# Optimization experiments

Measured on AMD Instinct MI355X. Metric: run time of the kernel, lower is better.

The kernel has to match this reference:

```python
import jax, jax.numpy as jnp
import numpy as np

B, C, T, V, P = 32, 64, 512, 54, 4
EPS = 1e-5


def setup_inputs() -> dict:
    key = jax.random.key(0)
    ks = jax.random.split(key, 5)
    x = jax.random.normal(ks[0], (B, C, T, V), dtype=jnp.float32)
    A = jax.random.uniform(ks[1], (P, V, V), dtype=jnp.float32)
    gweights = jax.random.normal(ks[2], (P, V, V), dtype=jnp.float32)
    W = jax.random.normal(ks[3], (P, C, C), dtype=jnp.float32) * 0.05  # (P, C_out, C_in)
    b = jax.random.normal(ks[4], (P, C), dtype=jnp.float32) * 0.05
    gamma = jnp.ones((C,), dtype=jnp.float32)
    beta = jnp.zeros((C,), dtype=jnp.float32)
    return {"x": x, "A": A, "gweights": gweights, "W": W, "b": b,
            "gamma": gamma, "beta": beta}


def reference(x, A, gweights, W, b, gamma, beta):
    # x: (B, C_in, T, V)
    Aeff = A * gweights  # (P, V, V), learned-weighted adjacency
    # per-part graph aggregation (x @ A_p) followed by 1x1 conv, summed over parts
    # out[b,o,t,v] = sum_p sum_c sum_u x[b,c,t,u] * Aeff[p,u,v] * W[p,o,c] + sum_p b[p,o]
    y = jnp.einsum('bctu,puv,poc->botv', x, Aeff, W, optimize=True)
    y = y + jnp.sum(b, axis=0)[None, :, None, None]
    # BatchNorm2d in training mode: batch stats over (B, T, V) per channel
    mean = jnp.mean(y, axis=(0, 2, 3), keepdims=True)
    var = jnp.mean(jnp.square(y - mean), axis=(0, 2, 3), keepdims=True)
    y = (y - mean) * jax.lax.rsqrt(var + EPS)
    y = y * gamma[None, :, None, None] + beta[None, :, None, None]
    y = jax.nn.relu(y)
    # temporal_conv is Identity (kernel_size=None); residual shortcut is Identity (C_in==C_out)
    return y + x
```

## Files before the change

### kernel.cpp

```cpp
#include <hip/hip_runtime.h>
#include <hip/hip_bf16.h>


typedef __bf16 bf16_t;
typedef __bf16 bf16x8 __attribute__((ext_vector_type(8)));
typedef __bf16 bf16x4 __attribute__((ext_vector_type(4)));
typedef float  f32x4  __attribute__((ext_vector_type(4)));
typedef unsigned int uint32;

static __device__ __forceinline__ f32x4 mfma16(bf16x8 a, bf16x8 b, f32x4 c) {
  return __builtin_amdgcn_mfma_f32_16x16x32_bf16(a, b, c, 0, 0, 0);
}
static __device__ __forceinline__ uint32 pk2(float a, float b) {
  union { __bf16 h; unsigned short u; } ua, ub;
  ua.h = (__bf16)a; ub.h = (__bf16)b;
  return (uint32)ua.u | ((uint32)ub.u << 16);
}

#define XTOT 56623104ull

__global__ __launch_bounds__(256) void k_prep(
    const float* __restrict__ A, const float* __restrict__ g,
    const float* __restrict__ W, const float* __restrict__ bias,
    bf16_t* __restrict__ W2, bf16_t* __restrict__ Ae,
    float* __restrict__ bsum, float* __restrict__ stats) {
  int i = blockIdx.x * 256 + threadIdx.x;
  if (i < 16384) {
    int o = i >> 8, k = i & 255, p = k >> 6, c = k & 63;
    W2[i] = (bf16_t)W[p * 4096 + o * 64 + c];
  }
  if (i < 224 * 64) {
    int pv = i >> 6, u = i & 63;
    int p = pv / 56, v = pv - p * 56;
    float val = 0.f;
    if (v < 54 && u < 54) {
      int idx = (p * 54 + u) * 54 + v;
      val = A[idx] * g[idx];
    }
    Ae[i] = (bf16_t)val;
  }
  if (i < 64) {
    float s = 0.f;
    for (int p = 0; p < 4; ++p) s += bias[p * 64 + i];
    bsum[i] = s;
  }
  if (i < 8192) stats[i] = 0.f;
}

#define ZS  264
#define XSS 72

template<bool YBF16>
__global__ __launch_bounds__(256, 3) void k_pass1(
    const float* __restrict__ x, const bf16_t* __restrict__ W2,
    const bf16_t* __restrict__ Ae, const float* __restrict__ bsum,
    void* __restrict__ yprev, float* __restrict__ stats) {
  __shared__ bf16_t Zt[64 * ZS];
  __shared__ bf16_t Xs[64 * XSS];

  const int tid  = threadIdx.x;
  const int bid  = blockIdx.x;
  const int b    = bid >> 7;
  const int t0   = (bid & 127) << 2;
  const int w    = tid >> 6;
  const int L    = tid & 63;
  const int quad = L >> 4;
  const int l15  = L & 15;

  for (int i = tid; i < 8 * ZS / 2; i += 256)
    ((uint32*)(Zt + 56 * ZS))[i] = 0u;

  bf16x8 wf[8];
  #pragma unroll
  for (int kk = 0; kk < 8; ++kk)
    wf[kk] = *(const bf16x8*)(W2 + (((w << 4) + l15) << 8) + (kk << 5) + (quad << 3));

  int zoff[14];
  #pragma unroll
  for (int n = 0; n < 14; ++n) {
    int pv = (n << 4) + l15;
    int p = pv / 56;
    int v = pv - p * 56;
    zoff[n] = v * ZS + (p << 6) + (w << 4) + (quad << 2);
  }

  const int oc  = (w << 4) + l15;
  const float bsv = bsum[oc];
  float ssum = 0.f, ssq = 0.f;

  const size_t LIM   = XTOT - 2;
  const size_t gbase = ((size_t)(b << 6) + (tid >> 5)) * 27648 + ((size_t)(tid & 31) << 1);
  uint32* xsd = (uint32*)((char*)Xs + (tid >> 5) * (XSS * 2) + ((tid & 31) << 2));

  float2 pf[8];
  #pragma unroll
  for (int j = 0; j < 8; ++j) {
    size_t a = gbase + (size_t)j * 221184 + (size_t)t0 * 54;
    if (a > LIM) a = LIM;
    pf[j] = *(const float2*)(x + a);
  }

  for (int tt = 0; tt < 4; ++tt) {
    const int t = t0 + tt;

    #pragma unroll
    for (int j = 0; j < 8; ++j) xsd[j * 288] = pk2(pf[j].x, pf[j].y);

    if (tt < 3) {
      #pragma unroll
      for (int j = 0; j < 8; ++j) {
        size_t a = gbase + (size_t)j * 221184 + (size_t)(t + 1) * 54;
        if (a > LIM) a = LIM;
        pf[j] = *(const float2*)(x + a);
      }
    }

    __syncthreads();

    const bf16_t* xr = Xs + oc * XSS;
    bf16x8 xa0 = *(const bf16x8*)(xr + (quad << 3));
    bf16x8 xa1 = *(const bf16x8*)(xr + 32 + (quad << 3));
    #pragma unroll
    for (int n = 0; n < 14; ++n) {
      const bf16_t* ar = Ae + (((n << 4) + l15) << 6) + (quad << 3);
      f32x4 acc = {0.f, 0.f, 0.f, 0.f};
      acc = mfma16(xa0, *(const bf16x8*)(ar), acc);
      acc = mfma16(xa1, *(const bf16x8*)(ar + 32), acc);
      uint32* dst = (uint32*)(Zt + zoff[n]);
      dst[0] = pk2(acc[0], acc[1]);
      dst[1] = pk2(acc[2], acc[3]);
    }

    __syncthreads();

    const size_t obase = (((size_t)((b << 6) + oc) << 9) + (size_t)t) * 54;
    #pragma unroll
    for (int mi = 0; mi < 4; ++mi) {
      f32x4 acc = {0.f, 0.f, 0.f, 0.f};
      #pragma unroll
      for (int kk = 0; kk < 8; ++kk) {
        bf16x8 za = *(const bf16x8*)(Zt + ((mi << 4) + l15) * ZS
                                        + (kk << 5) + (quad << 3));
        acc = mfma16(za, wf[kk], acc);
      }
      const int v0 = (mi << 4) + (quad << 2);
      if (v0 + 3 < 54) {
        float y0 = acc[0] + bsv, y1 = acc[1] + bsv, y2 = acc[2] + bsv, y3 = acc[3] + bsv;
        if (YBF16) {
          uint32* d = (uint32*)((bf16_t*)yprev + obase + v0);
          d[0] = pk2(y0, y1); d[1] = pk2(y2, y3);
        } else {
          float2* d = (float2*)((float*)yprev + obase + v0);
          d[0] = make_float2(y0, y1); d[1] = make_float2(y2, y3);
        }
        ssum += y0 + y1 + y2 + y3;
        ssq  += y0 * y0 + y1 * y1 + y2 * y2 + y3 * y3;
      } else if (v0 == 52) {
        float y0 = acc[0] + bsv, y1 = acc[1] + bsv;
        if (YBF16) {
          *(uint32*)((bf16_t*)yprev + obase + v0) = pk2(y0, y1);
        } else {
          *(float2*)((float*)yprev + obase + v0) = make_float2(y0, y1);
        }
        ssum += y0 + y1;
        ssq  += y0 * y0 + y1 * y1;
      }
    }
  }

  ssum += __shfl_xor(ssum, 16); ssq += __shfl_xor(ssq, 16);
  ssum += __shfl_xor(ssum, 32); ssq += __shfl_xor(ssq, 32);
  if (L < 16) {
    float* sb = stats + (bid & 63) * 128;
    atomicAdd(&sb[oc], ssum);
    atomicAdd(&sb[64 + oc], ssq);
  }
}

__global__ void k_finalize(const float* __restrict__ gamma, const float* __restrict__ beta,
                           const float* __restrict__ stats, float* __restrict__ ac) {
  int o = threadIdx.x;
  if (o >= 64) return;
  float S = 0.f, Q = 0.f;
  for (int buf = 0; buf < 64; ++buf) {
    S += stats[buf * 128 + o];
    Q += stats[buf * 128 + 64 + o];
  }
  const float inv = 1.0f / 884736.0f;
  float mean = S * inv;
  float var  = Q * inv - mean * mean;
  float a = gamma[o] * rsqrtf(var + 1e-5f);
  ac[o] = a;
  ac[64 + o] = beta[o] - mean * a;
}

template<bool YBF16>
__global__ __launch_bounds__(256) void k_pass2(const float* __restrict__ x,
                                               const float* __restrict__ ac,
                                               const void* __restrict__ yprev,
                                               float* __restrict__ out) {
  const int slab = blockIdx.y;
  const int o = slab & 63;
  const size_t base = (size_t)slab * 27648 + (size_t)(((blockIdx.x << 8) + threadIdx.x) << 2);
  const float a = ac[o], c = ac[64 + o];
  float y0, y1, y2, y3;
  if (YBF16) {
    bf16x4 yp = *(const bf16x4*)((const bf16_t*)yprev + base);
    y0 = (float)yp[0]; y1 = (float)yp[1]; y2 = (float)yp[2]; y3 = (float)yp[3];
  } else {
    float4 yp = *(const float4*)((const float*)yprev + base);
    y0 = yp.x; y1 = yp.y; y2 = yp.z; y3 = yp.w;
  }
  float4 xv = *(const float4*)(x + base);
  float4 r;
  r.x = fmaxf(fmaf(a, y0, c), 0.f) + xv.x;
  r.y = fmaxf(fmaf(a, y1, c), 0.f) + xv.y;
  r.z = fmaxf(fmaf(a, y2, c), 0.f) + xv.z;
  r.w = fmaxf(fmaf(a, y3, c), 0.f) + xv.w;
  *(float4*)(out + base) = r;
}

extern "C" void kernel_launch(void* const* d_in, const int* in_sizes, int n_in,
                              void* d_out, int out_size, void* d_ws, size_t ws_size,
                              hipStream_t stream) {
  const float* x     = (const float*)d_in[0];
  const float* A     = (const float*)d_in[1];
  const float* g     = (const float*)d_in[2];
  const float* W     = (const float*)d_in[3];
  const float* bias  = (const float*)d_in[4];
  const float* gamma = (const float*)d_in[5];
  const float* beta  = (const float*)d_in[6];

  char* ws = (char*)d_ws;
  bf16_t* W2    = (bf16_t*)(ws + 0);
  bf16_t* Ae    = (bf16_t*)(ws + 32768);
  float*  bsum  = (float*)(ws + 61440);
  float*  stats = (float*)(ws + 61696);
  float*  ac    = (float*)(ws + 94464);
  const size_t YP_OFF   = 98304;
  const size_t YP_BYTES = (size_t)32 * 64 * 512 * 54 * 2;
  float* out = (float*)d_out;

  k_prep<<<64, 256, 0, stream>>>(A, g, W, bias, W2, Ae, bsum, stats);

  if (ws_size >= YP_OFF + YP_BYTES + 4096) {
    bf16_t* ypre = (bf16_t*)(ws + YP_OFF);
    k_pass1<true><<<4096, 256, 0, stream>>>(x, W2, Ae, bsum, ypre, stats);
    k_finalize<<<1, 64, 0, stream>>>(gamma, beta, stats, ac);
    k_pass2<true><<<dim3(27, 2048), 256, 0, stream>>>(x, ac, ypre, out);
  } else {
    k_pass1<false><<<4096, 256, 0, stream>>>(x, W2, Ae, bsum, out, stats);
    k_finalize<<<1, 64, 0, stream>>>(gamma, beta, stats, ac);
    k_pass2<false><<<dim3(27, 2048), 256, 0, stream>>>(x, ac, out, out);
  }
}
```

Measured before the change: 757.8 us.

## Stage bf16 pre-norm output in LDS and write it block-contiguous

Pass1 now collects each timestep's bf16 pre-BN output in a shared tile and writes it to the workspace as one contiguous block-ordered chunk with 16-byte stores, instead of scattered 8-byte stores across channel rows. Pass2 is rewritten to read that block-linear layout contiguously and to gather x and scatter out by index, with the BN coefficients cached in LDS. The x prefetch now masks out the idle lanes instead of clamping addresses, and it is issued after the second barrier rather than before the first. The aim is better coalescing of the intermediate traffic. The cost is an extra barrier per timestep, integer divides in pass2, and strided 8-byte accesses to x and out there.

```diff
diff --git a/kernel.cpp b/kernel.cpp
--- a/kernel.cpp
+++ b/kernel.cpp
@@ -16,8 +16,12 @@
   ua.h = (__bf16)a; ub.h = (__bf16)b;
   return (uint32)ua.u | ((uint32)ub.u << 16);
 }
-
-#define XTOT 56623104ull
+static __device__ __forceinline__ float bflo(uint32 u) {
+  union { uint32 u; float f; } r; r.u = u << 16; return r.f;
+}
+static __device__ __forceinline__ float bfhi(uint32 u) {
+  union { uint32 u; float f; } r; r.u = u & 0xffff0000u; return r.f;
+}
 
 __global__ __launch_bounds__(256) void k_prep(
     const float* __restrict__ A, const float* __restrict__ g,
@@ -57,6 +61,7 @@
     void* __restrict__ yprev, float* __restrict__ stats) {
   __shared__ bf16_t Zt[64 * ZS];
   __shared__ bf16_t Xs[64 * XSS];
+  __shared__ __align__(16) bf16_t Ys[64 * 54];
 
   const int tid  = threadIdx.x;
   const int bid  = blockIdx.x;
@@ -88,16 +93,18 @@
   const float bsv = bsum[oc];
   float ssum = 0.f, ssq = 0.f;
 
-  const size_t LIM   = XTOT - 2;
-  const size_t gbase = ((size_t)(b << 6) + (tid >> 5)) * 27648 + ((size_t)(tid & 31) << 1);
-  uint32* xsd = (uint32*)((char*)Xs + (tid >> 5) * (XSS * 2) + ((tid & 31) << 2));
+  const int  f2   = tid & 31;
+  const bool ldon = f2 < 27;
+  const size_t gbase = ((size_t)(b << 6) + (tid >> 5)) * 27648 + ((size_t)f2 << 1);
+  uint32* xsd = (uint32*)((char*)Xs + (tid >> 5) * (XSS * 2) + (f2 << 2));
 
   float2 pf[8];
   #pragma unroll
-  for (int j = 0; j < 8; ++j) {
-    size_t a = gbase + (size_t)j * 221184 + (size_t)t0 * 54;
-    if (a > LIM) a = LIM;
-    pf[j] = *(const float2*)(x + a);
+  for (int j = 0; j < 8; ++j) pf[j] = make_float2(0.f, 0.f);
+  if (ldon) {
+    #pragma unroll
+    for (int j = 0; j < 8; ++j)
+      pf[j] = *(const float2*)(x + gbase + (size_t)j * 221184 + (size_t)t0 * 54);
   }
 
   for (int tt = 0; tt < 4; ++tt) {
@@ -105,15 +112,6 @@
 
     #pragma unroll
     for (int j = 0; j < 8; ++j) xsd[j * 288] = pk2(pf[j].x, pf[j].y);
-
-    if (tt < 3) {
-      #pragma unroll
-      for (int j = 0; j < 8; ++j) {
-        size_t a = gbase + (size_t)j * 221184 + (size_t)(t + 1) * 54;
-        if (a > LIM) a = LIM;
-        pf[j] = *(const float2*)(x + a);
-      }
-    }
 
     __syncthreads();
 
@@ -132,6 +130,12 @@
     }
 
     __syncthreads();
+
+    if (ldon && tt < 3) {
+      #pragma unroll
+      for (int j = 0; j < 8; ++j)
+        pf[j] = *(const float2*)(x + gbase + (size_t)j * 221184 + (size_t)(t + 1) * 54);
+    }
 
     const size_t obase = (((size_t)((b << 6) + oc) << 9) + (size_t)t) * 54;
     #pragma unroll
@@ -147,7 +151,7 @@
       if (v0 + 3 < 54) {
         float y0 = acc[0] + bsv, y1 = acc[1] + bsv, y2 = acc[2] + bsv, y3 = acc[3] + bsv;
         if (YBF16) {
-          uint32* d = (uint32*)((bf16_t*)yprev + obase + v0);
+          uint32* d = (uint32*)(Ys + oc * 54 + v0);
           d[0] = pk2(y0, y1); d[1] = pk2(y2, y3);
         } else {
           float2* d = (float2*)((float*)yprev + obase + v0);
@@ -158,13 +162,23 @@
       } else if (v0 == 52) {
         float y0 = acc[0] + bsv, y1 = acc[1] + bsv;
         if (YBF16) {
-          *(uint32*)((bf16_t*)yprev + obase + v0) = pk2(y0, y1);
+          *(uint32*)(Ys + oc * 54 + v0) = pk2(y0, y1);
         } else {
           *(float2*)((float*)yprev + obase + v0) = make_float2(y0, y1);
         }
         ssum += y0 + y1;
         ssq  += y0 * y0 + y1 * y1;
       }
+    }
+
+    if (YBF16) {
+      __syncthreads();
+      const uint4* ys4 = (const uint4*)Ys;
+      uint4* yp4 = (uint4*)((uint32*)yprev + (size_t)bid * 6912 + (size_t)tt * 1728);
+      yp4[tid] = ys4[tid];
+      if (tid < 176) yp4[256 + tid] = ys4[256 + tid];
+    } else {
+      __syncthreads();
     }
   }
 
@@ -194,29 +208,55 @@
   ac[64 + o] = beta[o] - mean * a;
 }
 
-template<bool YBF16>
-__global__ __launch_bounds__(256) void k_pass2(const float* __restrict__ x,
-                                               const float* __restrict__ ac,
-                                               const void* __restrict__ yprev,
-                                               float* __restrict__ out) {
+__global__ __launch_bounds__(256) void k_pass2_lin(
+    const float* __restrict__ x, const float* __restrict__ ac,
+    const void* __restrict__ yprev, float* __restrict__ out) {
+  __shared__ float acS[128];
+  const int tid = threadIdx.x;
+  const int bid = blockIdx.x;
+  if (tid < 128) acS[tid] = ac[tid];
+  __syncthreads();
+
+  const int b  = bid >> 7;
+  const int t0 = (bid & 127) << 2;
+  const uint32* yp = (const uint32*)yprev + (size_t)bid * 6912;
+  const float* xb  = x + (size_t)b * 1769472;
+  float* ob        = out + (size_t)b * 1769472;
+
+  #pragma unroll 3
+  for (int k = 0; k < 27; ++k) {
+    const int d  = (k << 8) + tid;
+    const int e0 = d << 1;
+    const unsigned tt = (unsigned)e0 / 3456u;
+    const unsigned r  = (unsigned)e0 - tt * 3456u;
+    const unsigned ocv = r / 54u;
+    const unsigned v   = r - ocv * 54u;
+    const uint32 u = yp[d];
+    const float a = acS[ocv], cc = acS[64 + ocv];
+    const size_t xi = (size_t)ocv * 27648 + (size_t)(t0 + tt) * 54 + v;
+    const float2 xv = *(const float2*)(xb + xi);
+    float2 o2;
+    o2.x = fmaxf(fmaf(a, bflo(u), cc), 0.f) + xv.x;
+    o2.y = fmaxf(fmaf(a, bfhi(u), cc), 0.f) + xv.y;
+    *(float2*)(ob + xi) = o2;
+  }
+}
+
+__global__ __launch_bounds__(256) void k_pass2_fb(const float* __restrict__ x,
+                                                  const float* __restrict__ ac,
+                                                  const float* __restrict__ yprev,
+                                                  float* __restrict__ out) {
   const int slab = blockIdx.y;
   const int o = slab & 63;
   const size_t base = (size_t)slab * 27648 + (size_t)(((blockIdx.x << 8) + threadIdx.x) << 2);
   const float a = ac[o], c = ac[64 + o];
-  float y0, y1, y2, y3;
-  if (YBF16) {
-    bf16x4 yp = *(const bf16x4*)((const bf16_t*)yprev + base);
-    y0 = (float)yp[0]; y1 = (float)yp[1]; y2 = (float)yp[2]; y3 = (float)yp[3];
-  } else {
-    float4 yp = *(const float4*)((const float*)yprev + base);
-    y0 = yp.x; y1 = yp.y; y2 = yp.z; y3 = yp.w;
-  }
+  float4 yp = *(const float4*)(yprev + base);
   float4 xv = *(const float4*)(x + base);
   float4 r;
-  r.x = fmaxf(fmaf(a, y0, c), 0.f) + xv.x;
-  r.y = fmaxf(fmaf(a, y1, c), 0.f) + xv.y;
-  r.z = fmaxf(fmaf(a, y2, c), 0.f) + xv.z;
-  r.w = fmaxf(fmaf(a, y3, c), 0.f) + xv.w;
+  r.x = fmaxf(fmaf(a, yp.x, c), 0.f) + xv.x;
+  r.y = fmaxf(fmaf(a, yp.y, c), 0.f) + xv.y;
+  r.z = fmaxf(fmaf(a, yp.z, c), 0.f) + xv.z;
+  r.w = fmaxf(fmaf(a, yp.w, c), 0.f) + xv.w;
   *(float4*)(out + base) = r;
 }
 
@@ -247,10 +287,10 @@
     bf16_t* ypre = (bf16_t*)(ws + YP_OFF);
     k_pass1<true><<<4096, 256, 0, stream>>>(x, W2, Ae, bsum, ypre, stats);
     k_finalize<<<1, 64, 0, stream>>>(gamma, beta, stats, ac);
-    k_pass2<true><<<dim3(27, 2048), 256, 0, stream>>>(x, ac, ypre, out);
+    k_pass2_lin<<<4096, 256, 0, stream>>>(x, ac, ypre, out);
   } else {
     k_pass1<false><<<4096, 256, 0, stream>>>(x, W2, Ae, bsum, out, stats);
     k_finalize<<<1, 64, 0, stream>>>(gamma, beta, stats, ac);
-    k_pass2<false><<<dim3(27, 2048), 256, 0, stream>>>(x, ac, out, out);
-  }
-}
+    k_pass2_fb<<<dim3(27, 2048), 256, 0, stream>>>(x, ac, out, out);
+  }
+}
```

Result: slower. 784.1 us (+3.5%).
